# Optimization experiments

Measured on AMD Instinct MI355X. Metric: run time of the kernel, lower is better.

The kernel has to match this reference:

```python
import jax, jax.numpy as jnp
import numpy as np

IMAGE_SIZE = 224  # self.image_size; dims are all equal to this so postprocess is one bilinear resize
EPS = 1e-12      # F.normalize default eps


def setup_inputs() -> dict:
    key = jax.random.key(0)
    k1, k2 = jax.random.split(key)
    embeddings = jax.random.normal(k1, (2, 9, 256, 48, 48), dtype=jnp.float32)
    # binary class masks in {0,1}; channel 0 (background) is recomputed inside forward
    prompt_masks = jax.random.randint(k2, (2, 8, 4, 48, 48), 0, 2).astype(jnp.float32)
    dims = jnp.full((2, 1, 2), IMAGE_SIZE, dtype=jnp.int32)  # all original sizes == image_size
    return {"embeddings": embeddings, "prompt_masks": prompt_masks, "dims": dims}


def reference(embeddings, prompt_masks, dims):
    B, M, D, H, W = embeddings.shape
    HW = H * W
    q = embeddings[:, 0]            # (B, D, H, W)  query
    s = embeddings[:, 1:]           # (B, M-1, D, H, W)  supports
    # F.normalize: x / max(||x||, eps) along the feature dim
    qn = q / jnp.maximum(jnp.sqrt(jnp.sum(q * q, axis=1, keepdims=True)), EPS)
    sn = s / jnp.maximum(jnp.sqrt(jnp.sum(s * s, axis=2, keepdims=True)), EPS)

    q2 = qn.reshape(B, D, HW).transpose(0, 2, 1)              # (B, Q, D)
    s2 = sn.reshape(B, M - 1, D, HW).transpose(0, 1, 3, 2)    # (B, M1, K, D)
    sim = jnp.einsum('bqd,bmkd->bqmk', q2, s2)                # (B, Q, M1, K) cosine sims

    # nearest-resize of prompt masks to compare_size==(H,W) is identity here (same size)
    N = prompt_masks.shape[2]
    pm = prompt_masks.reshape(B, M - 1, N, HW)
    background = (pm[:, :, 1:, :].sum(axis=2) == 0).astype(sim.dtype)  # (B, M1, HW)
    pm = pm.at[:, :, 0, :].set(background)

    neg_inf = jnp.array(-jnp.inf, sim.dtype)
    logits = []
    for n in range(N):  # small fixed class count
        cm = pm[:, :, n, :][:, None]                 # (B, 1, M1, K) broadcast over Q
        masked = jnp.where(cm == 0, neg_inf, sim)    # (B, Q, M1, K)
        logits.append(masked.reshape(B, HW, -1).max(axis=-1))  # (B, Q)
    logits = jnp.stack(logits, axis=1).reshape(B, N, H, W)

    # postprocess_masks: bilinear to image_size; all original sizes == image_size so the
    # per-image second interpolate is identity and padding amounts are zero.
    out = jax.image.resize(logits, (B, N, IMAGE_SIZE, IMAGE_SIZE), method='bilinear')
    # masks[:,0][masks[:,0]==-inf] = 0  (no-op here, kept for faithfulness)
    out = out.at[:, 0].set(jnp.where(jnp.isneginf(out[:, 0]), 0.0, out[:, 0]))
    return out
```

## Files before the change

### kernel.cpp

```cpp
#include <hip/hip_runtime.h>
#include <hip/hip_bf16.h>
#include <math.h>

#define BB 2
#define MM 9
#define MS 8
#define DD 256
#define HW 2304
#define NCLS 4
#define OUTR 224

typedef float floatx4 __attribute__((ext_vector_type(4)));
typedef __bf16 bf16x8 __attribute__((ext_vector_type(8)));
typedef unsigned short ushortx8 __attribute__((ext_vector_type(8)));

__device__ __forceinline__ unsigned enc_f(float f) {
    unsigned u = __float_as_uint(f);
    return (u & 0x80000000u) ? ~u : (u | 0x80000000u);
}
__device__ __forceinline__ float dec_f(unsigned k) {
    unsigned u = (k & 0x80000000u) ? (k & 0x7FFFFFFFu) : ~k;
    return __uint_as_float(u);
}

__global__ __launch_bounds__(256) void knorm(const float* __restrict__ emb,
                                             __hip_bfloat16* __restrict__ outp,
                                             unsigned* __restrict__ enc_logits) {
    __shared__ float tile[256][33];
    __shared__ float psum[8][32];
    __shared__ float sscale[32];
    const int bm   = blockIdx.y;
    const int pix0 = blockIdx.x * 32;
    const int tid  = threadIdx.x;

    int flat = (blockIdx.y * gridDim.x + blockIdx.x) * 256 + tid;
    if (flat < BB * NCLS * HW) enc_logits[flat] = 0u;

    const float* src = emb + (size_t)bm * DD * HW + pix0;
    {
        const int dr = tid >> 3;
        const int p4 = (tid & 7) * 4;
#pragma unroll
        for (int r = 0; r < 8; ++r) {
            int d = r * 32 + dr;
            floatx4 v = *(const floatx4*)(src + (size_t)d * HW + p4);
            float* t = &tile[d][p4];
            t[0] = v[0]; t[1] = v[1]; t[2] = v[2]; t[3] = v[3];
        }
    }
    __syncthreads();
    {
        const int pc = tid & 31;
        const int dr = tid >> 5;
        float ss = 0.f;
#pragma unroll
        for (int s = 0; s < 32; ++s) {
            float v = tile[dr * 32 + s][pc];
            ss += v * v;
        }
        psum[dr][pc] = ss;
    }
    __syncthreads();
    if (tid < 32) {
        float t = 0.f;
#pragma unroll
        for (int c = 0; c < 8; ++c) t += psum[c][tid];
        sscale[tid] = 1.0f / fmaxf(sqrtf(t), 1e-12f);
    }
    __syncthreads();
    unsigned* dstu = (unsigned*)(outp + (size_t)bm * HW * DD + (size_t)pix0 * DD);
    const int d2 = tid & 127;
    const int ph = tid >> 7;
#pragma unroll
    for (int it = 0; it < 16; ++it) {
        int p = it * 2 + ph;
        float sc = sscale[p];
        float v0 = tile[2 * d2][p] * sc;
        float v1 = tile[2 * d2 + 1][p] * sc;
        unsigned pack = ((unsigned)__bfloat16_as_ushort(__float2bfloat16(v1)) << 16) |
                        (unsigned)__bfloat16_as_ushort(__float2bfloat16(v0));
        dstu[(size_t)p * 128 + d2] = pack;
    }
}

__device__ __forceinline__ void gld16(const unsigned short* g, unsigned short* l) {
    __builtin_amdgcn_global_load_lds((__attribute__((address_space(1))) void*)g,
                                     (__attribute__((address_space(3))) void*)l, 16, 0, 0);
}

#define BK 32
#define REDSTRIDE 132
#define SMEM_BYTES 33792

__global__ __launch_bounds__(256, 4) void kgemm(const unsigned short* __restrict__ normed,
                                                const float* __restrict__ pm,
                                                unsigned* __restrict__ enc_logits) {
    __shared__ __attribute__((aligned(16))) unsigned char smem[SMEM_BYTES];
    unsigned short* const S0 = (unsigned short*)smem;
    float* red = (float*)smem;

    const int ct = blockIdx.x;
    const int rt = blockIdx.y;
    const int b  = blockIdx.z;
    const int m  = ct / 18;
    const int kt = ct % 18;

    const int tid  = threadIdx.x;
    const int lane = tid & 63;
    const int wave = tid >> 6;
    const int wr = wave >> 1, wc = wave & 1;
    const int lrow = lane & 15;
    const int quad = lane >> 4;

    const unsigned short* A  = normed + (size_t)(b * MM) * (HW * DD) + (size_t)(rt * 128) * DD;
    const unsigned short* Bp = normed + (size_t)(b * MM + 1 + m) * (HW * DD) + (size_t)(kt * 128) * DD;

    const float* pmB = pm + (size_t)(b * MS + m) * NCLS * HW;
    int mj[4];
#pragma unroll
    for (int j = 0; j < 4; ++j) {
        int kp = kt * 128 + wc * 64 + j * 16 + lrow;
        float p1 = pmB[HW + kp], p2 = pmB[2 * HW + kp], p3 = pmB[3 * HW + kp];
        mj[j] = ((p1 + p2 + p3 == 0.0f) ? 1 : 0) | (p1 != 0.0f ? 2 : 0) |
                (p2 != 0.0f ? 4 : 0) | (p3 != 0.0f ? 8 : 0);
    }

    const int srq  = lane >> 2;
    const int scol = ((lane & 3) ^ ((srq >> 1) & 3)) * 8;
    const unsigned short* gA = A  + (size_t)(wave * 32 + srq) * DD + scol;
    const unsigned short* gB = Bp + (size_t)(wave * 32 + srq) * DD + scol;

    floatx4 zero = {0.f, 0.f, 0.f, 0.f};
    floatx4 acc[4][4];
#pragma unroll
    for (int i = 0; i < 4; ++i)
#pragma unroll
        for (int j = 0; j < 4; ++j) acc[i][j] = zero;

#pragma unroll
    for (int q = 0; q < 2; ++q) {
        gld16(gA + (size_t)(q * 16) * DD, S0 +        (wave * 2 + q) * 512);
        gld16(gB + (size_t)(q * 16) * DD, S0 + 4096 + (wave * 2 + q) * 512);
    }
    __syncthreads();

    const int pc8 = (quad ^ ((lrow >> 1) & 3)) * 8;

#pragma unroll
    for (int t = 0; t < DD / BK; ++t) {
        const int cb = t & 1;
        unsigned short* const Ac = S0 + cb * 8192;
        unsigned short* const Bc = Ac + 4096;
        if (t < DD / BK - 1) {
            unsigned short* const An = S0 + (cb ^ 1) * 8192;
#pragma unroll
            for (int q = 0; q < 2; ++q) {
                gld16(gA + (size_t)(q * 16) * DD + (t + 1) * BK, An +        (wave * 2 + q) * 512);
                gld16(gB + (size_t)(q * 16) * DD + (t + 1) * BK, An + 4096 + (wave * 2 + q) * 512);
            }
        }
        bf16x8 af[4], bfr[4];
#pragma unroll
        for (int i = 0; i < 4; ++i) {
            int ar = wr * 64 + i * 16 + lrow;
            int br = wc * 64 + i * 16 + lrow;
            af[i]  = __builtin_bit_cast(bf16x8, *(const ushortx8*)(Ac + ar * 32 + pc8));
            bfr[i] = __builtin_bit_cast(bf16x8, *(const ushortx8*)(Bc + br * 32 + pc8));
        }
#pragma unroll
        for (int i = 0; i < 4; ++i)
#pragma unroll
            for (int j = 0; j < 4; ++j)
                acc[i][j] = __builtin_amdgcn_mfma_f32_16x16x32_bf16(af[i], bfr[j], acc[i][j], 0, 0, 0);
        __syncthreads();
    }

    const int col32 = wc * 16 + lrow;

#pragma unroll
    for (int p = 0; p < 2; ++p) {
        if (p) __syncthreads();
        bool bit[2][4];
#pragma unroll
        for (int nn = 0; nn < 2; ++nn) {
            int n = p * 2 + nn;
#pragma unroll
            for (int j = 0; j < 4; ++j) bit[nn][j] = (mj[j] >> n) & 1;
        }
#pragma unroll
        for (int nn = 0; nn < 2; ++nn) {
#pragma unroll
            for (int i = 0; i < 4; ++i) {
                floatx4 o;
#pragma unroll
                for (int r = 0; r < 4; ++r) {
                    float t0 = bit[nn][0] ? acc[i][0][r] : -INFINITY;
                    float t1 = bit[nn][1] ? acc[i][1][r] : -INFINITY;
                    float t2 = bit[nn][2] ? acc[i][2][r] : -INFINITY;
                    float t3 = bit[nn][3] ? acc[i][3][r] : -INFINITY;
                    o[r] = fmaxf(fmaxf(t0, t1), fmaxf(t2, t3));
                }
                int rowbase = wr * 64 + i * 16 + quad * 4;
                *(floatx4*)(red + ((size_t)(nn * 32 + col32)) * REDSTRIDE + rowbase) = o;
            }
        }
        __syncthreads();
        {
            int nn  = tid >> 7;
            int row = tid & 127;
            float v = -INFINITY;
#pragma unroll
            for (int c = 0; c < 32; ++c)
                v = fmaxf(v, red[((size_t)(nn * 32 + c)) * REDSTRIDE + row]);
            int n = p * 2 + nn;
            atomicMax(enc_logits + ((size_t)b * NCLS + n) * HW + rt * 128 + row, enc_f(v));
        }
    }
}

__global__ __launch_bounds__(256) void kresize(const unsigned* __restrict__ enc_logits,
                                               float* __restrict__ out) {
    int idx = blockIdx.x * 256 + threadIdx.x;
    if (idx >= BB * NCLS * OUTR * OUTR) return;
    int ox = idx % OUTR;
    int oy = (idx / OUTR) % OUTR;
    int bn = idx / (OUTR * OUTR);
    const unsigned* src = enc_logits + (size_t)bn * HW;
    const float inv = 48.0f / 224.0f;
    float sx = (ox + 0.5f) * inv - 0.5f;
    float sy = (oy + 0.5f) * inv - 0.5f;
    int x0 = (int)floorf(sx); float fx = sx - x0;
    int y0 = (int)floorf(sy); float fy = sy - y0;
    int x0c = min(max(x0, 0), 47), x1c = min(max(x0 + 1, 0), 47);
    int y0c = min(max(y0, 0), 47), y1c = min(max(y0 + 1, 0), 47);
    float v00 = dec_f(src[y0c * 48 + x0c]), v01 = dec_f(src[y0c * 48 + x1c]);
    float v10 = dec_f(src[y1c * 48 + x0c]), v11 = dec_f(src[y1c * 48 + x1c]);
    float v = (1.f - fy) * ((1.f - fx) * v00 + fx * v01) + fy * ((1.f - fx) * v10 + fx * v11);
    if ((bn & 3) == 0 && v == -INFINITY) v = 0.f;
    out[idx] = v;
}

extern "C" void kernel_launch(void* const* d_in, const int* in_sizes, int n_in,
                              void* d_out, int out_size, void* d_ws, size_t ws_size,
                              hipStream_t stream) {
    const float* emb = (const float*)d_in[0];
    const float* pm  = (const float*)d_in[1];
    float* out = (float*)d_out;

    char* ws = (char*)d_ws;
    const size_t normed_bytes = (size_t)BB * MM * HW * DD * 2;
    __hip_bfloat16* normed = (__hip_bfloat16*)(ws);
    unsigned*       enc    = (unsigned*)(ws + normed_bytes);

    knorm<<<dim3(HW / 32, BB * MM), 256, 0, stream>>>(emb, normed, enc);
    kgemm<<<dim3(144, 18, BB), 256, 0, stream>>>((const unsigned short*)normed, pm, enc);
    kresize<<<(BB * NCLS * OUTR * OUTR + 255) / 256, 256, 0, stream>>>(enc, out);
}
```

Before: 144.3 us.

## Fuse norm, GEMM and resize into one persistent cooperative kernel

The three kernels are merged into one persistent cooperative kernel. Blocks loop over the norm tiles, then the GEMM tiles, then the resize elements, with grid-wide syncs between phases. This removes two kernel launches and the gaps between them. In exchange it adds grid sync overhead and uses a fixed grid of occupancy times 256 blocks, so it may balance load worse than the original grid. Shared memory is unified, and the original three launches remain as a fallback.

```diff
diff --git a/kernel.cpp b/kernel.cpp
--- a/kernel.cpp
+++ b/kernel.cpp
@@ -1,6 +1,9 @@
 #include <hip/hip_runtime.h>
+#include <hip/hip_cooperative_groups.h>
 #include <hip/hip_bf16.h>
 #include <math.h>
+
+namespace cg = cooperative_groups;
 
 #define BB 2
 #define MM 9
@@ -9,6 +12,11 @@
 #define HW 2304
 #define NCLS 4
 #define OUTR 224
+#define NCT 144
+#define NRT 18
+#define NTILE_GEMM (NCT * NRT * BB)
+#define NTILE_NORM ((HW / 32) * (BB * MM))
+#define NOUT (BB * NCLS * OUTR * OUTR)
 
 typedef float floatx4 __attribute__((ext_vector_type(4)));
 typedef __bf16 bf16x8 __attribute__((ext_vector_type(8)));
@@ -23,18 +31,22 @@
     return __uint_as_float(u);
 }
 
-__global__ __launch_bounds__(256) void knorm(const float* __restrict__ emb,
-                                             __hip_bfloat16* __restrict__ outp,
-                                             unsigned* __restrict__ enc_logits) {
-    __shared__ float tile[256][33];
-    __shared__ float psum[8][32];
-    __shared__ float sscale[32];
-    const int bm   = blockIdx.y;
-    const int pix0 = blockIdx.x * 32;
-    const int tid  = threadIdx.x;
-
-    int flat = (blockIdx.y * gridDim.x + blockIdx.x) * 256 + tid;
-    if (flat < BB * NCLS * HW) enc_logits[flat] = 0u;
+__device__ __forceinline__ void gld16(const unsigned short* g, unsigned short* l) {
+    __builtin_amdgcn_global_load_lds((__attribute__((address_space(1))) void*)g,
+                                     (__attribute__((address_space(3))) void*)l, 16, 0, 0);
+}
+
+#define BK 32
+#define REDSTRIDE 132
+#define SMEM_BYTES 34944
+
+
+__device__ __forceinline__ void norm_tile_body(const float* __restrict__ emb,
+                                               __hip_bfloat16* __restrict__ outp,
+                                               unsigned char* smem, int bm, int pix0, int tid) {
+    float* tile   = (float*)smem;
+    float* psum   = (float*)(smem + 33792);
+    float* sscale = (float*)(smem + 34816);
 
     const float* src = emb + (size_t)bm * DD * HW + pix0;
     {
@@ -44,27 +56,27 @@
         for (int r = 0; r < 8; ++r) {
             int d = r * 32 + dr;
             floatx4 v = *(const floatx4*)(src + (size_t)d * HW + p4);
-            float* t = &tile[d][p4];
+            float* t = &tile[d * 33 + p4];
             t[0] = v[0]; t[1] = v[1]; t[2] = v[2]; t[3] = v[3];
         }
     }
     __syncthreads();
     {
-        const int pc = tid & 31;
-        const int dr = tid >> 5;
+        const int pc  = tid & 31;
+        const int dr8 = tid >> 5;
         float ss = 0.f;
 #pragma unroll
         for (int s = 0; s < 32; ++s) {
-            float v = tile[dr * 32 + s][pc];
+            float v = tile[(s * 8 + dr8) * 33 + pc];
             ss += v * v;
         }
-        psum[dr][pc] = ss;
+        psum[dr8 * 32 + pc] = ss;
     }
     __syncthreads();
     if (tid < 32) {
         float t = 0.f;
 #pragma unroll
-        for (int c = 0; c < 8; ++c) t += psum[c][tid];
+        for (int c = 0; c < 8; ++c) t += psum[c * 32 + tid];
         sscale[tid] = 1.0f / fmaxf(sqrtf(t), 1e-12f);
     }
     __syncthreads();
@@ -75,37 +87,24 @@
     for (int it = 0; it < 16; ++it) {
         int p = it * 2 + ph;
         float sc = sscale[p];
-        float v0 = tile[2 * d2][p] * sc;
-        float v1 = tile[2 * d2 + 1][p] * sc;
+        float v0 = tile[(2 * d2) * 33 + p] * sc;
+        float v1 = tile[(2 * d2 + 1) * 33 + p] * sc;
         unsigned pack = ((unsigned)__bfloat16_as_ushort(__float2bfloat16(v1)) << 16) |
                         (unsigned)__bfloat16_as_ushort(__float2bfloat16(v0));
         dstu[(size_t)p * 128 + d2] = pack;
     }
 }
 
-__device__ __forceinline__ void gld16(const unsigned short* g, unsigned short* l) {
-    __builtin_amdgcn_global_load_lds((__attribute__((address_space(1))) void*)g,
-                                     (__attribute__((address_space(3))) void*)l, 16, 0, 0);
-}
-
-#define BK 32
-#define REDSTRIDE 132
-#define SMEM_BYTES 33792
-
-__global__ __launch_bounds__(256, 4) void kgemm(const unsigned short* __restrict__ normed,
-                                                const float* __restrict__ pm,
-                                                unsigned* __restrict__ enc_logits) {
-    __shared__ __attribute__((aligned(16))) unsigned char smem[SMEM_BYTES];
+__device__ __forceinline__ void gemm_tile_body(const unsigned short* __restrict__ normed,
+                                               const float* __restrict__ pm,
+                                               unsigned* __restrict__ enc_logits,
+                                               unsigned char* smem,
+                                               int b, int rt, int ct, int tid) {
     unsigned short* const S0 = (unsigned short*)smem;
     float* red = (float*)smem;
 
-    const int ct = blockIdx.x;
-    const int rt = blockIdx.y;
-    const int b  = blockIdx.z;
     const int m  = ct / 18;
     const int kt = ct % 18;
-
-    const int tid  = threadIdx.x;
     const int lane = tid & 63;
     const int wave = tid >> 6;
     const int wr = wave >> 1, wc = wave & 1;
@@ -176,7 +175,6 @@
     }
 
     const int col32 = wc * 16 + lrow;
-
 #pragma unroll
     for (int p = 0; p < 2; ++p) {
         if (p) __syncthreads();
@@ -218,10 +216,8 @@
     }
 }
 
-__global__ __launch_bounds__(256) void kresize(const unsigned* __restrict__ enc_logits,
-                                               float* __restrict__ out) {
-    int idx = blockIdx.x * 256 + threadIdx.x;
-    if (idx >= BB * NCLS * OUTR * OUTR) return;
+__device__ __forceinline__ void resize_body(const unsigned* __restrict__ enc_logits,
+                                            float* __restrict__ out, int idx) {
     int ox = idx % OUTR;
     int oy = (idx / OUTR) % OUTR;
     int bn = idx / (OUTR * OUTR);
@@ -240,6 +236,63 @@
     out[idx] = v;
 }
 
+__global__ __launch_bounds__(256, 4) void kfused(const float* __restrict__ emb,
+                                                 const float* __restrict__ pm,
+                                                 float* __restrict__ out,
+                                                 __hip_bfloat16* __restrict__ normed,
+                                                 unsigned* __restrict__ enc) {
+    __shared__ __attribute__((aligned(16))) unsigned char smem[SMEM_BYTES];
+    const int tid = threadIdx.x;
+    cg::grid_group grid = cg::this_grid();
+
+    {
+        int flat = blockIdx.x * 256 + tid;
+        if (flat < BB * NCLS * HW) enc[flat] = 0u;
+        for (int tI = blockIdx.x; tI < NTILE_NORM; tI += gridDim.x) {
+            __syncthreads();
+            norm_tile_body(emb, normed, smem, tI / 72, (tI % 72) * 32, tid);
+        }
+    }
+    grid.sync();
+    {
+        const unsigned short* nrm = (const unsigned short*)normed;
+        for (int g = blockIdx.x; g < NTILE_GEMM; g += gridDim.x) {
+            const int ct = g % NCT;
+            const int rt = (g / NCT) % NRT;
+            const int b  = g / (NCT * NRT);
+            __syncthreads();
+            gemm_tile_body(nrm, pm, enc, smem, b, rt, ct, tid);
+        }
+    }
+    grid.sync();
+    for (int idx = blockIdx.x * 256 + tid; idx < NOUT; idx += gridDim.x * 256)
+        resize_body(enc, out, idx);
+}
+
+__global__ __launch_bounds__(256) void knorm(const float* __restrict__ emb,
+                                             __hip_bfloat16* __restrict__ outp,
+                                             unsigned* __restrict__ enc_logits) {
+    __shared__ __attribute__((aligned(16))) unsigned char smem[SMEM_BYTES];
+    const int tid = threadIdx.x;
+    int flat = (blockIdx.y * gridDim.x + blockIdx.x) * 256 + tid;
+    if (flat < BB * NCLS * HW) enc_logits[flat] = 0u;
+    norm_tile_body(emb, outp, smem, blockIdx.y, blockIdx.x * 32, tid);
+}
+
+__global__ __launch_bounds__(256, 4) void kgemm(const unsigned short* __restrict__ normed,
+                                                const float* __restrict__ pm,
+                                                unsigned* __restrict__ enc_logits) {
+    __shared__ __attribute__((aligned(16))) unsigned char smem[SMEM_BYTES];
+    gemm_tile_body(normed, pm, enc_logits, smem, blockIdx.z, blockIdx.y, blockIdx.x, threadIdx.x);
+}
+
+__global__ __launch_bounds__(256) void kresize(const unsigned* __restrict__ enc_logits,
+                                               float* __restrict__ out) {
+    int idx = blockIdx.x * 256 + threadIdx.x;
+    if (idx >= NOUT) return;
+    resize_body(enc_logits, out, idx);
+}
+
 extern "C" void kernel_launch(void* const* d_in, const int* in_sizes, int n_in,
                               void* d_out, int out_size, void* d_ws, size_t ws_size,
                               hipStream_t stream) {
@@ -252,7 +305,21 @@
     __hip_bfloat16* normed = (__hip_bfloat16*)(ws);
     unsigned*       enc    = (unsigned*)(ws + normed_bytes);
 
-    knorm<<<dim3(HW / 32, BB * MM), 256, 0, stream>>>(emb, normed, enc);
-    kgemm<<<dim3(144, 18, BB), 256, 0, stream>>>((const unsigned short*)normed, pm, enc);
-    kresize<<<(BB * NCLS * OUTR * OUTR + 255) / 256, 256, 0, stream>>>(enc, out);
-}
+    static int nblk = 0;
+    if (nblk == 0) {
+        int mb = 0;
+        hipError_t e = hipOccupancyMaxActiveBlocksPerMultiprocessor(&mb, (const void*)kfused, 256, 0);
+        if (e != hipSuccess || mb < 1) mb = 1;
+        if (mb > 4) mb = 4;
+        nblk = mb * 256;
+    }
+
+    void* args[] = {(void*)&emb, (void*)&pm, (void*)&out, (void*)&normed, (void*)&enc};
+    hipError_t le = hipLaunchCooperativeKernel((const void*)kfused, dim3(nblk), dim3(256),
+                                               args, 0, stream);
+    if (le != hipSuccess) {
+        knorm<<<dim3(HW / 32, BB * MM), 256, 0, stream>>>(emb, normed, enc);
+        kgemm<<<dim3(NCT, NRT, BB), 256, 0, stream>>>((const unsigned short*)normed, pm, enc);
+        kresize<<<(NOUT + 255) / 256, 256, 0, stream>>>(enc, out);
+    }
+}
```

Measured after the change: 307.3 us. +113.0%, slower.
